# Performance work log

Measured on AMD Instinct MI355X. Metric: run time of the kernel, lower is better.

Reference implementation:

```python
import jax, jax.numpy as jnp
import numpy as np

B, C, D_MODEL, N_HEADS = 2, 2048, 1024, 16


def rotary_matrix(context_length: int, d: int) -> jnp.ndarray:
    """Faithful vectorization of get_rotary_matrix: theta = 10000^(-2*(i-1)/d)."""
    half = d // 2
    i = jnp.arange(half, dtype=jnp.float32)
    theta = 10000.0 ** (-2.0 * (i - 1.0) / d)          # note the (i-1), as in source
    m = jnp.arange(context_length, dtype=jnp.float32)
    ang = m[:, None] * theta                            # [C, d/2]
    c, s = jnp.cos(ang), jnp.sin(ang)
    ev = 2 * jnp.arange(half)
    od = ev + 1
    R = jnp.zeros((context_length, d, d), jnp.float32)
    R = R.at[:, ev, ev].set(c)
    R = R.at[:, ev, od].set(-s)
    R = R.at[:, od, ev].set(s)
    R = R.at[:, od, od].set(c)
    return R


def setup_inputs() -> dict:
    key = jax.random.key(0)
    k1, k2, k3, k4 = jax.random.split(key, 4)
    x = jax.random.normal(k1, (B, C, D_MODEL), dtype=jnp.float32)
    w_qkv = jax.random.normal(k2, (3 * D_MODEL, D_MODEL), dtype=jnp.float32) * 0.02
    w_out = jax.random.normal(k3, (D_MODEL, D_MODEL), dtype=jnp.float32) * 0.02
    b_out = jax.random.normal(k4, (D_MODEL,), dtype=jnp.float32) * 0.02
    return {"x": x, "w_qkv": w_qkv, "w_out": w_out, "b_out": b_out}


def reference(x, w_qkv, w_out, b_out):
    b, c, d = x.shape
    h = N_HEADS
    dh = d // h
    qkv = x @ w_qkv.T                                   # [B,C,3D]
    q, k, v = jnp.split(qkv, 3, axis=-1)
    # [B,C,D] -> [B,H,C,dh]
    q = q.reshape(b, c, h, dh).transpose(0, 2, 1, 3)
    k = k.reshape(b, c, h, dh).transpose(0, 2, 1, 3)
    v = v.reshape(b, c, h, dh).transpose(0, 2, 1, 3)
    R = rotary_matrix(c, dh)                            # [C,dh,dh]
    q_rot = jnp.einsum('bhci,cij->bhcj', q, R)
    k_rot = jnp.einsum('bhci,cij->bhcj', k, R)
    scale = jnp.sqrt(jnp.float32(dh))
    # exact math of the source: exp with no max subtraction, separate num/den
    attn_num = jnp.exp(jnp.einsum('bhqd,bhkd->bhqk', q_rot, k_rot) / scale)
    attn_den = jnp.exp(jnp.einsum('bhqd,bhkd->bhqk', q, k) / scale)
    attn_den = jnp.sum(attn_den, axis=-1, keepdims=True)
    attn = attn_num / attn_den
    causal = jnp.tril(jnp.ones((c, c), jnp.float32))[None, None]
    attn = jnp.where(causal == 0, 0.0, attn)
    y = jnp.einsum('bhqk,bhkd->bhqd', attn, v)
    y = y.transpose(0, 2, 1, 3).reshape(b, c, d)
    return y @ w_out.T + b_out
```

## Files before the change

### kernel.cpp

```cpp
#include <hip/hip_runtime.h>
#include <math.h>
#include <stdint.h>

#define BB 2
#define CC 2048
#define DD 1024
#define HH 16
#define DHH 64
#define HALF 32

typedef __attribute__((ext_vector_type(8))) short bf16x8;
typedef __attribute__((ext_vector_type(4))) float f32x4;
typedef unsigned int u32;

#define EXPC 0.1803368801f

__device__ __forceinline__ ushort f2bf(float f) {
    uint32_t u = __builtin_bit_cast(uint32_t, f);
    u = (u + 0x7FFFu + ((u >> 16) & 1u)) >> 16;
    return (ushort)u;
}

__device__ __forceinline__ void gload16(const void* g, void* lds) {
    __builtin_amdgcn_global_load_lds(
        (const u32 __attribute__((address_space(1)))*)g,
        (u32 __attribute__((address_space(3)))*)lds, 16, 0, 0);
}

__global__ __launch_bounds__(256) void cast3_k(const float* __restrict__ x,
                                               const float* __restrict__ wq,
                                               const float* __restrict__ wo,
                                               ushort* __restrict__ xb,
                                               ushort* __restrict__ wqb,
                                               ushort* __restrict__ wob) {
    int id = blockIdx.x * 256 + threadIdx.x;
    const float* s;
    ushort* d;
    int off;
    if (id < 524288)       { s = x;  d = xb;  off = id; }
    else if (id < 917504)  { s = wq; d = wqb; off = id - 524288; }
    else                   { s = wo; d = wob; off = id - 917504; }
    float4 a = *reinterpret_cast<const float4*>(s + (size_t)off * 8);
    float4 b = *reinterpret_cast<const float4*>(s + (size_t)off * 8 + 4);
    bf16x8 o;
    o[0] = (short)f2bf(a.x); o[1] = (short)f2bf(a.y);
    o[2] = (short)f2bf(a.z); o[3] = (short)f2bf(a.w);
    o[4] = (short)f2bf(b.x); o[5] = (short)f2bf(b.y);
    o[6] = (short)f2bf(b.z); o[7] = (short)f2bf(b.w);
    *reinterpret_cast<bf16x8*>(d + (size_t)off * 8) = o;
}

__global__ __launch_bounds__(256) void rope_table_k(float* __restrict__ ct, float* __restrict__ st) {
    int idx = blockIdx.x * 256 + threadIdx.x;
    if (idx >= CC * HALF) return;
    int m = idx >> 5;
    int t = idx & 31;
    double theta_d = pow(10000.0, -2.0 * ((double)t - 1.0) / 64.0);
    float theta = (float)theta_d;
    float ang = (float)m * theta;
    ct[idx] = cosf(ang);
    st[idx] = sinf(ang);
}

__global__ __launch_bounds__(256) void qkv_gemm_mfma_k(const ushort* __restrict__ xb,
                                                       const ushort* __restrict__ wqb,
                                                       const float* __restrict__ ct,
                                                       const float* __restrict__ st,
                                                       ushort* __restrict__ q,
                                                       ushort* __restrict__ k,
                                                       ushort* __restrict__ qr,
                                                       ushort* __restrict__ kr,
                                                       ushort* __restrict__ vT3) {
    __shared__ ushort Al[128 * 64];
    __shared__ ushort Bl[128 * 64];
    const int tid = threadIdx.x;
    const int w = tid >> 6, l = tid & 63;
    const int l15 = l & 15, lg = l >> 4;
    const int wr = w >> 1, wc = w & 1;
    const int m0 = blockIdx.x * 128, n0 = blockIdx.y * 128;
    const int lrow = l >> 3, lch = l & 7;

    f32x4 acc[4][4];
#pragma unroll
    for (int i = 0; i < 4; i++)
#pragma unroll
        for (int j = 0; j < 4; j++) acc[i][j] = (f32x4){0.f, 0.f, 0.f, 0.f};

    for (int k0 = 0; k0 < 1024; k0 += 64) {
        __syncthreads();
#pragma unroll
        for (int c = 0; c < 4; c++) {
            int row = w * 32 + c * 8 + lrow;
            int gch = (lch ^ (row & 7)) * 8;
            gload16(xb + (size_t)(m0 + row) * 1024 + k0 + gch, &Al[(w * 32 + c * 8) * 64]);
            gload16(wqb + (size_t)(n0 + row) * 1024 + k0 + gch, &Bl[(w * 32 + c * 8) * 64]);
        }
        __syncthreads();
#pragma unroll
        for (int kk = 0; kk < 2; kk++) {
            bf16x8 a[4], b[4];
#pragma unroll
            for (int mt = 0; mt < 4; mt++) {
                int row = wr * 64 + mt * 16 + l15;
                a[mt] = *reinterpret_cast<const bf16x8*>(&Al[row * 64 + ((kk * 4 + lg) ^ (row & 7)) * 8]);
            }
#pragma unroll
            for (int nt = 0; nt < 4; nt++) {
                int row = wc * 64 + nt * 16 + l15;
                b[nt] = *reinterpret_cast<const bf16x8*>(&Bl[row * 64 + ((kk * 4 + lg) ^ (row & 7)) * 8]);
            }
#pragma unroll
            for (int mt = 0; mt < 4; mt++)
#pragma unroll
                for (int nt = 0; nt < 4; nt++)
                    acc[mt][nt] = __builtin_amdgcn_mfma_f32_16x16x32_bf16(a[mt], b[nt], acc[mt][nt], 0, 0, 0);
        }
    }
#pragma unroll
    for (int mt = 0; mt < 4; mt++)
#pragma unroll
        for (int nt = 0; nt < 4; nt++) {
            int n = n0 + wc * 64 + nt * 16 + l15;
            int part = n >> 10;
            int d = n & 1023;
            int h = d >> 6, dd = d & 63;
            int mbase = m0 + wr * 64 + mt * 16 + lg * 4;
            int bb = mbase >> 11, cpos = mbase & 2047;
            if (part == 2) {
                int kt = cpos >> 6, kcol = cpos & 63;
                ushort4 pk;
                pk.x = f2bf(acc[mt][nt][0]); pk.y = f2bf(acc[mt][nt][1]);
                pk.z = f2bf(acc[mt][nt][2]); pk.w = f2bf(acc[mt][nt][3]);
                size_t off = ((((size_t)(bb * HH + h)) * 32 + kt) * 64 + dd) * 64 + kcol;
                *reinterpret_cast<ushort4*>(vT3 + off) = pk;
            } else {
                ushort* dstu = (part == 0) ? q : k;
                ushort* dstr = (part == 0) ? qr : kr;
                const float sgn = (dd & 1) ? -1.f : 1.f;
                const int t = dd >> 1;
#pragma unroll
                for (int r = 0; r < 4; r++) {
                    float val = acc[mt][nt][r];
                    float par = __shfl_xor(val, 1, 64);
                    float c = ct[(cpos + r) * 32 + t];
                    float s = st[(cpos + r) * 32 + t];
                    float rot = val * c + sgn * par * s;
                    size_t base = (((size_t)bb * HH + h) * CC + (cpos + r)) * DHH + dd;
                    dstu[base] = f2bf(val);
                    dstr[base] = f2bf(rot);
                }
            }
        }
}

__global__ __launch_bounds__(256) void den_k(const ushort* __restrict__ qg,
                                             const ushort* __restrict__ kg,
                                             float* __restrict__ deng) {
    __shared__ ushort Kd[2][128 * 64];
    const int tid = threadIdx.x;
    const int w = tid >> 6, l = tid & 63;
    const int l15 = l & 15, lg = l >> 4;
    const int lrow = l >> 3, lch = l & 7;
    const int bh = blockIdx.y;
    const int q0 = blockIdx.x * 64;
    const ushort* qb = qg + (size_t)bh * CC * DHH;
    const ushort* kb = kg + (size_t)bh * CC * DHH;

    bf16x8 qf[2];
#pragma unroll
    for (int kk = 0; kk < 2; kk++) {
        int row = q0 + w * 16 + l15;
        qf[kk] = *reinterpret_cast<const bf16x8*>(qb + (size_t)row * DHH + kk * 32 + lg * 8);
    }

    float dacc[2] = {0.f, 0.f};

#define DSTAGE(KT, BUF)                                                                     \
    {                                                                                       \
        const int sk0 = (KT) * 128;                                                         \
        _Pragma("unroll")                                                                   \
        for (int c = 0; c < 4; c++) {                                                       \
            int row = w * 32 + c * 8 + lrow;                                                \
            int gch = (lch ^ (row & 7)) * 8;                                                \
            gload16(kb + (size_t)(sk0 + row) * DHH + gch, &Kd[BUF][(w * 32 + c * 8) * 64]); \
        }                                                                                   \
    }

    DSTAGE(0, 0);
    __syncthreads();
    int cur = 0;

    for (int kt = 0; kt < 16; kt++) {
        if (kt < 15) DSTAGE(kt + 1, cur ^ 1);
#pragma unroll
        for (int nt = 0; nt < 8; nt++) {
            f32x4 s = (f32x4){0.f, 0.f, 0.f, 0.f};
#pragma unroll
            for (int kk = 0; kk < 2; kk++) {
                int krow = nt * 16 + l15;
                bf16x8 ka = *reinterpret_cast<const bf16x8*>(
                    &Kd[cur][krow * 64 + ((kk * 4 + lg) ^ (krow & 7)) * 8]);
                s = __builtin_amdgcn_mfma_f32_16x16x32_bf16(ka, qf[kk], s, 0, 0, 0);
            }
#pragma unroll
            for (int r = 0; r < 4; r++)
                dacc[nt & 1] += __builtin_amdgcn_exp2f(s[r] * EXPC);
        }
        __syncthreads();
        cur ^= 1;
    }
    float d = dacc[0] + dacc[1];
    d += __shfl_xor(d, 16, 64);
    d += __shfl_xor(d, 32, 64);
    if (lg == 0)
        deng[(size_t)bh * CC + q0 + w * 16 + l15] = d;
#undef DSTAGE
}

__global__ __launch_bounds__(256, 2) void attn_pair_k(const ushort* __restrict__ vT3,
                                                      const ushort* __restrict__ qrg,
                                                      const ushort* __restrict__ krg,
                                                      const float* __restrict__ deng,
                                                      ushort* __restrict__ y) {
    __shared__ ushort Krl[2][64 * 64];
    __shared__ ushort Pl[4][16 * 64];

    const int tid = threadIdx.x;
    const int w = tid >> 6, l = tid & 63;
    const int l15 = l & 15, lg = l >> 4;
    const int lrow = l >> 3, lch = l & 7;

    const int bid = blockIdx.x;
    const int xcd = bid & 7;
    const int idx = bid >> 3;
    const int sub = idx & 3;
    const int tp = idx >> 2;
    const int bh = xcd * 4 + sub;
    const int q0a = tp * 64;
    const int NB = 31 - tp;
    const int q0b = NB * 64;

    const ushort* qrb = qrg + (size_t)bh * CC * DHH;
    const ushort* krb = krg + (size_t)bh * CC * DHH;
    const ushort* vtb = vT3 + (size_t)bh * 32 * 64 * 64;

    bf16x8 qrfA[2], qrfB[2];
#pragma unroll
    for (int kk = 0; kk < 2; kk++) {
        qrfA[kk] = *reinterpret_cast<const bf16x8*>(qrb + (size_t)(q0a + w * 16 + l15) * DHH + kk * 32 + lg * 8);
        qrfB[kk] = *reinterpret_cast<const bf16x8*>(qrb + (size_t)(q0b + w * 16 + l15) * DHH + kk * 32 + lg * 8);
    }

    f32x4 yaccA[4], yaccB[4];
#pragma unroll
    for (int nt = 0; nt < 4; nt++) {
        yaccA[nt] = (f32x4){0.f, 0.f, 0.f, 0.f};
        yaccB[nt] = (f32x4){0.f, 0.f, 0.f, 0.f};
    }

#define STAGE(KT, BUF)                                                                         \
    {                                                                                          \
        const int sk0 = (KT) * 64;                                                             \
        _Pragma("unroll")                                                                      \
        for (int c = 0; c < 2; c++) {                                                          \
            int row = w * 16 + c * 8 + lrow;                                                   \
            int gch = (lch ^ (row & 7)) * 8;                                                   \
            gload16(krb + (size_t)(sk0 + row) * DHH + gch, &Krl[BUF][(w * 16 + c * 8) * 64]);  \
        }                                                                                      \
    }

#define NUMPV(Q0, QRF, YACC, LASTKT)                                                           \
    {                                                                                          \
        const bool diag = (kt == (LASTKT));                                                    \
        const int qrow = (Q0) + w * 16 + l15;                                                  \
        _Pragma("unroll")                                                                      \
        for (int nt = 0; nt < 4; nt++) {                                                       \
            f32x4 s = (f32x4){0.f, 0.f, 0.f, 0.f};                                             \
            _Pragma("unroll")                                                                  \
            for (int kk = 0; kk < 2; kk++) {                                                   \
                int krow = nt * 16 + l15;                                                      \
                bf16x8 ka = *reinterpret_cast<const bf16x8*>(                                  \
                    &Krl[cur][krow * 64 + ((kk * 4 + lg) ^ (krow & 7)) * 8]);                  \
                s = __builtin_amdgcn_mfma_f32_16x16x32_bf16(ka, (QRF)[kk], s, 0, 0, 0);        \
            }                                                                                  \
            float pe[4];                                                                       \
            _Pragma("unroll")                                                                  \
            for (int r = 0; r < 4; r++)                                                        \
                pe[r] = __builtin_amdgcn_exp2f(s[r] * EXPC);                                   \
            if (diag) {                                                                        \
                _Pragma("unroll")                                                              \
                for (int r = 0; r < 4; r++) {                                                  \
                    int key = kt * 64 + nt * 16 + lg * 4 + r;                                  \
                    pe[r] = (key <= qrow) ? pe[r] : 0.f;                                       \
                }                                                                              \
            }                                                                                  \
            u32 pk0, pk1;                                                                      \
            asm("v_cvt_pk_bf16_f32 %0, %1, %2" : "=v"(pk0) : "v"(pe[0]), "v"(pe[1]));          \
            asm("v_cvt_pk_bf16_f32 %0, %1, %2" : "=v"(pk1) : "v"(pe[2]), "v"(pe[3]));          \
            int swzc = (nt * 2 + (lg >> 1)) ^ (l15 & 7);                                       \
            uint2 pr; pr.x = pk0; pr.y = pk1;                                                  \
            *reinterpret_cast<uint2*>(&Pl[w][l15 * 64 + swzc * 8 + (lg & 1) * 4]) = pr;        \
        }                                                                                      \
        bf16x8 pa[2];                                                                          \
        _Pragma("unroll")                                                                      \
        for (int kk2 = 0; kk2 < 2; kk2++) {                                                    \
            int rc = (kk2 * 4 + lg) ^ (l15 & 7);                                               \
            pa[kk2] = *reinterpret_cast<const bf16x8*>(&Pl[w][l15 * 64 + rc * 8]);             \
        }                                                                                      \
        _Pragma("unroll")                                                                      \
        for (int nt2 = 0; nt2 < 4; nt2++)                                                      \
            _Pragma("unroll")                                                                  \
            for (int kk2 = 0; kk2 < 2; kk2++)                                                  \
                (YACC)[nt2] = __builtin_amdgcn_mfma_f32_16x16x32_bf16(pa[kk2], vf[nt2][kk2],   \
                                                                      (YACC)[nt2], 0, 0, 0);   \
    }

    STAGE(0, 0);
    __syncthreads();
    int cur = 0;

    for (int kt = 0; kt <= NB; kt++) {
        bf16x8 vf[4][2];
        const ushort* vt0 = vtb + (size_t)kt * 64 * 64;
#pragma unroll
        for (int nt2 = 0; nt2 < 4; nt2++)
#pragma unroll
            for (int kk2 = 0; kk2 < 2; kk2++)
                vf[nt2][kk2] = *reinterpret_cast<const bf16x8*>(
                    vt0 + (nt2 * 16 + l15) * 64 + kk2 * 32 + lg * 8);

        if (kt < NB) STAGE(kt + 1, cur ^ 1);

        if (kt <= tp) NUMPV(q0a, qrfA, yaccA, tp);
        NUMPV(q0b, qrfB, yaccB, NB);

        __syncthreads();
        cur ^= 1;
    }

    const int b = bh >> 4, h = bh & 15;
#pragma unroll
    for (int r = 0; r < 4; r++) {
        int rowA = q0a + w * 16 + lg * 4 + r;
        int rowB = q0b + w * 16 + lg * 4 + r;
        float invA = 1.f / deng[(size_t)bh * CC + rowA];
        float invB = 1.f / deng[(size_t)bh * CC + rowB];
#pragma unroll
        for (int nt2 = 0; nt2 < 4; nt2++) {
            y[((size_t)b * CC + rowA) * DD + h * DHH + nt2 * 16 + l15] = f2bf(yaccA[nt2][r] * invA);
            y[((size_t)b * CC + rowB) * DD + h * DHH + nt2 * 16 + l15] = f2bf(yaccB[nt2][r] * invB);
        }
    }
#undef STAGE
#undef NUMPV
}

__global__ __launch_bounds__(256) void out_proj_mfma_k(const ushort* __restrict__ yb,
                                                       const ushort* __restrict__ wob,
                                                       const float* __restrict__ bias,
                                                       float* __restrict__ out) {
    __shared__ ushort Al[128 * 64];
    __shared__ ushort Bl[128 * 64];
    const int tid = threadIdx.x;
    const int w = tid >> 6, l = tid & 63;
    const int l15 = l & 15, lg = l >> 4;
    const int wr = w >> 1, wc = w & 1;
    const int m0 = blockIdx.x * 128, n0 = blockIdx.y * 128;
    const int lrow = l >> 3, lch = l & 7;

    f32x4 acc[4][4];
#pragma unroll
    for (int i = 0; i < 4; i++)
#pragma unroll
        for (int j = 0; j < 4; j++) acc[i][j] = (f32x4){0.f, 0.f, 0.f, 0.f};

    for (int k0 = 0; k0 < 1024; k0 += 64) {
        __syncthreads();
#pragma unroll
        for (int c = 0; c < 4; c++) {
            int row = w * 32 + c * 8 + lrow;
            int gch = (lch ^ (row & 7)) * 8;
            gload16(yb + (size_t)(m0 + row) * 1024 + k0 + gch, &Al[(w * 32 + c * 8) * 64]);
            gload16(wob + (size_t)(n0 + row) * 1024 + k0 + gch, &Bl[(w * 32 + c * 8) * 64]);
        }
        __syncthreads();
#pragma unroll
        for (int kk = 0; kk < 2; kk++) {
            bf16x8 a[4], b[4];
#pragma unroll
            for (int mt = 0; mt < 4; mt++) {
                int row = wr * 64 + mt * 16 + l15;
                a[mt] = *reinterpret_cast<const bf16x8*>(&Al[row * 64 + ((kk * 4 + lg) ^ (row & 7)) * 8]);
            }
#pragma unroll
            for (int nt = 0; nt < 4; nt++) {
                int row = wc * 64 + nt * 16 + l15;
                b[nt] = *reinterpret_cast<const bf16x8*>(&Bl[row * 64 + ((kk * 4 + lg) ^ (row & 7)) * 8]);
            }
#pragma unroll
            for (int mt = 0; mt < 4; mt++)
#pragma unroll
                for (int nt = 0; nt < 4; nt++)
                    acc[mt][nt] = __builtin_amdgcn_mfma_f32_16x16x32_bf16(a[mt], b[nt], acc[mt][nt], 0, 0, 0);
        }
    }
#pragma unroll
    for (int mt = 0; mt < 4; mt++)
#pragma unroll
        for (int nt = 0; nt < 4; nt++) {
            int n = n0 + wc * 64 + nt * 16 + l15;
            float bv = bias[n];
#pragma unroll
            for (int r = 0; r < 4; r++) {
                int m = m0 + wr * 64 + mt * 16 + lg * 4 + r;
                out[(size_t)m * 1024 + n] = acc[mt][nt][r] + bv;
            }
        }
}

extern "C" void kernel_launch(void* const* d_in, const int* in_sizes, int n_in,
                              void* d_out, int out_size, void* d_ws, size_t ws_size,
                              hipStream_t stream) {
    (void)in_sizes; (void)n_in; (void)out_size; (void)ws_size;
    const float* x     = (const float*)d_in[0];
    const float* w_qkv = (const float*)d_in[1];
    const float* w_out = (const float*)d_in[2];
    const float* b_out = (const float*)d_in[3];
    float* out = (float*)d_out;

    char* p = (char*)d_ws;
    float* ct = (float*)p;  p += (size_t)CC * HALF * 4;
    float* st = (float*)p;  p += (size_t)CC * HALF * 4;
    ushort* xb  = (ushort*)p; p += (size_t)4096 * 1024 * 2;
    ushort* wqb = (ushort*)p; p += (size_t)3072 * 1024 * 2;
    ushort* wob = (ushort*)p; p += (size_t)1024 * 1024 * 2;
    const size_t TEN = (size_t)BB * HH * CC * DHH;
    ushort* qb = (ushort*)p; p += TEN * 2;
    ushort* kb = (ushort*)p; p += TEN * 2;
    ushort* vT = (ushort*)p; p += TEN * 2;
    ushort* qr = (ushort*)p; p += TEN * 2;
    ushort* kr = (ushort*)p; p += TEN * 2;
    ushort* yb = (ushort*)p; p += (size_t)4096 * 1024 * 2;
    float* den = (float*)p;  p += (size_t)32 * CC * 4;

    cast3_k<<<dim3(4096), dim3(256), 0, stream>>>(x, w_qkv, w_out, xb, wqb, wob);
    rope_table_k<<<dim3((CC * HALF) / 256), dim3(256), 0, stream>>>(ct, st);
    qkv_gemm_mfma_k<<<dim3(32, 24), dim3(256), 0, stream>>>(xb, wqb, ct, st, qb, kb, qr, kr, vT);
    den_k<<<dim3(32, 32), dim3(256), 0, stream>>>(qb, kb, den);
    attn_pair_k<<<dim3(512), dim3(256), 0, stream>>>(vT, qr, kr, den, yb);
    out_proj_mfma_k<<<dim3(32, 8), dim3(256), 0, stream>>>(yb, wob, b_out, out);
}
```

Before: 176.1 us.

## Fuse denominator computation into paired causal attention kernel

Removes the separate den_k kernel and computes the unmasked softmax denominator inside the attention kernel. Each block now walks all 32 key tiles, staging both unrotated K and rotated K into LDS and accumulating exp sums for both query tiles. The denominators are reduced and broadcast in registers, so no global den buffer is needed. The change also adds s_setprio around MFMA groups and raises launch bounds to 4 blocks per SM. The cost is more LDS per block, more registers and longer per-block loops.

Result: slower. 264.7 us (+50.3%).

```diff
diff --git a/kernel.cpp b/kernel.cpp
--- a/kernel.cpp
+++ b/kernel.cpp
@@ -153,75 +153,13 @@
         }
 }
 
-__global__ __launch_bounds__(256) void den_k(const ushort* __restrict__ qg,
-                                             const ushort* __restrict__ kg,
-                                             float* __restrict__ deng) {
-    __shared__ ushort Kd[2][128 * 64];
-    const int tid = threadIdx.x;
-    const int w = tid >> 6, l = tid & 63;
-    const int l15 = l & 15, lg = l >> 4;
-    const int lrow = l >> 3, lch = l & 7;
-    const int bh = blockIdx.y;
-    const int q0 = blockIdx.x * 64;
-    const ushort* qb = qg + (size_t)bh * CC * DHH;
-    const ushort* kb = kg + (size_t)bh * CC * DHH;
-
-    bf16x8 qf[2];
-#pragma unroll
-    for (int kk = 0; kk < 2; kk++) {
-        int row = q0 + w * 16 + l15;
-        qf[kk] = *reinterpret_cast<const bf16x8*>(qb + (size_t)row * DHH + kk * 32 + lg * 8);
-    }
-
-    float dacc[2] = {0.f, 0.f};
-
-#define DSTAGE(KT, BUF)                                                                     \
-    {                                                                                       \
-        const int sk0 = (KT) * 128;                                                         \
-        _Pragma("unroll")                                                                   \
-        for (int c = 0; c < 4; c++) {                                                       \
-            int row = w * 32 + c * 8 + lrow;                                                \
-            int gch = (lch ^ (row & 7)) * 8;                                                \
-            gload16(kb + (size_t)(sk0 + row) * DHH + gch, &Kd[BUF][(w * 32 + c * 8) * 64]); \
-        }                                                                                   \
-    }
-
-    DSTAGE(0, 0);
-    __syncthreads();
-    int cur = 0;
-
-    for (int kt = 0; kt < 16; kt++) {
-        if (kt < 15) DSTAGE(kt + 1, cur ^ 1);
-#pragma unroll
-        for (int nt = 0; nt < 8; nt++) {
-            f32x4 s = (f32x4){0.f, 0.f, 0.f, 0.f};
-#pragma unroll
-            for (int kk = 0; kk < 2; kk++) {
-                int krow = nt * 16 + l15;
-                bf16x8 ka = *reinterpret_cast<const bf16x8*>(
-                    &Kd[cur][krow * 64 + ((kk * 4 + lg) ^ (krow & 7)) * 8]);
-                s = __builtin_amdgcn_mfma_f32_16x16x32_bf16(ka, qf[kk], s, 0, 0, 0);
-            }
-#pragma unroll
-            for (int r = 0; r < 4; r++)
-                dacc[nt & 1] += __builtin_amdgcn_exp2f(s[r] * EXPC);
-        }
-        __syncthreads();
-        cur ^= 1;
-    }
-    float d = dacc[0] + dacc[1];
-    d += __shfl_xor(d, 16, 64);
-    d += __shfl_xor(d, 32, 64);
-    if (lg == 0)
-        deng[(size_t)bh * CC + q0 + w * 16 + l15] = d;
-#undef DSTAGE
-}
-
-__global__ __launch_bounds__(256, 2) void attn_pair_k(const ushort* __restrict__ vT3,
-                                                      const ushort* __restrict__ qrg,
-                                                      const ushort* __restrict__ krg,
-                                                      const float* __restrict__ deng,
-                                                      ushort* __restrict__ y) {
+__global__ __launch_bounds__(256, 4) void attn_fused_k(const ushort* __restrict__ vT3,
+                                                       const ushort* __restrict__ qg,
+                                                       const ushort* __restrict__ kg,
+                                                       const ushort* __restrict__ qrg,
+                                                       const ushort* __restrict__ krg,
+                                                       ushort* __restrict__ y) {
+    __shared__ ushort Kl[2][64 * 64];
     __shared__ ushort Krl[2][64 * 64];
     __shared__ ushort Pl[4][16 * 64];
 
@@ -236,19 +174,25 @@
     const int sub = idx & 3;
     const int tp = idx >> 2;
     const int bh = xcd * 4 + sub;
+    const int NB = 31 - tp;
     const int q0a = tp * 64;
-    const int NB = 31 - tp;
     const int q0b = NB * 64;
 
+    const ushort* qb  = qg  + (size_t)bh * CC * DHH;
+    const ushort* kb  = kg  + (size_t)bh * CC * DHH;
     const ushort* qrb = qrg + (size_t)bh * CC * DHH;
     const ushort* krb = krg + (size_t)bh * CC * DHH;
     const ushort* vtb = vT3 + (size_t)bh * 32 * 64 * 64;
 
-    bf16x8 qrfA[2], qrfB[2];
+    bf16x8 qfA[2], qfB[2], qrfA[2], qrfB[2];
 #pragma unroll
     for (int kk = 0; kk < 2; kk++) {
-        qrfA[kk] = *reinterpret_cast<const bf16x8*>(qrb + (size_t)(q0a + w * 16 + l15) * DHH + kk * 32 + lg * 8);
-        qrfB[kk] = *reinterpret_cast<const bf16x8*>(qrb + (size_t)(q0b + w * 16 + l15) * DHH + kk * 32 + lg * 8);
+        int ra = q0a + w * 16 + l15;
+        int rb = q0b + w * 16 + l15;
+        qfA[kk]  = *reinterpret_cast<const bf16x8*>(qb  + (size_t)ra * DHH + kk * 32 + lg * 8);
+        qfB[kk]  = *reinterpret_cast<const bf16x8*>(qb  + (size_t)rb * DHH + kk * 32 + lg * 8);
+        qrfA[kk] = *reinterpret_cast<const bf16x8*>(qrb + (size_t)ra * DHH + kk * 32 + lg * 8);
+        qrfB[kk] = *reinterpret_cast<const bf16x8*>(qrb + (size_t)rb * DHH + kk * 32 + lg * 8);
     }
 
     f32x4 yaccA[4], yaccB[4];
@@ -257,6 +201,7 @@
         yaccA[nt] = (f32x4){0.f, 0.f, 0.f, 0.f};
         yaccB[nt] = (f32x4){0.f, 0.f, 0.f, 0.f};
     }
+    float daccA0 = 0.f, daccA1 = 0.f, daccB0 = 0.f, daccB1 = 0.f;
 
 #define STAGE(KT, BUF)                                                                         \
     {                                                                                          \
@@ -265,7 +210,9 @@
         for (int c = 0; c < 2; c++) {                                                          \
             int row = w * 16 + c * 8 + lrow;                                                   \
             int gch = (lch ^ (row & 7)) * 8;                                                   \
-            gload16(krb + (size_t)(sk0 + row) * DHH + gch, &Krl[BUF][(w * 16 + c * 8) * 64]);  \
+            gload16(kb + (size_t)(sk0 + row) * DHH + gch, &Kl[BUF][(w * 16 + c * 8) * 64]);    \
+            if ((KT) <= NB)                                                                    \
+                gload16(krb + (size_t)(sk0 + row) * DHH + gch, &Krl[BUF][(w * 16 + c * 8) * 64]); \
         }                                                                                      \
     }
 
@@ -275,14 +222,17 @@
         const int qrow = (Q0) + w * 16 + l15;                                                  \
         _Pragma("unroll")                                                                      \
         for (int nt = 0; nt < 4; nt++) {                                                       \
+            bf16x8 kra0, kra1;                                                                 \
+            {                                                                                  \
+                int krow = nt * 16 + l15;                                                      \
+                kra0 = *reinterpret_cast<const bf16x8*>(&Krl[cur][krow * 64 + ((0 + lg) ^ (krow & 7)) * 8]); \
+                kra1 = *reinterpret_cast<const bf16x8*>(&Krl[cur][krow * 64 + ((4 + lg) ^ (krow & 7)) * 8]); \
+            }                                                                                  \
+            __builtin_amdgcn_s_setprio(1);                                                     \
             f32x4 s = (f32x4){0.f, 0.f, 0.f, 0.f};                                             \
-            _Pragma("unroll")                                                                  \
-            for (int kk = 0; kk < 2; kk++) {                                                   \
-                int krow = nt * 16 + l15;                                                      \
-                bf16x8 ka = *reinterpret_cast<const bf16x8*>(                                  \
-                    &Krl[cur][krow * 64 + ((kk * 4 + lg) ^ (krow & 7)) * 8]);                  \
-                s = __builtin_amdgcn_mfma_f32_16x16x32_bf16(ka, (QRF)[kk], s, 0, 0, 0);        \
-            }                                                                                  \
+            s = __builtin_amdgcn_mfma_f32_16x16x32_bf16(kra0, (QRF)[0], s, 0, 0, 0);           \
+            s = __builtin_amdgcn_mfma_f32_16x16x32_bf16(kra1, (QRF)[1], s, 0, 0, 0);           \
+            __builtin_amdgcn_s_setprio(0);                                                     \
             float pe[4];                                                                       \
             _Pragma("unroll")                                                                  \
             for (int r = 0; r < 4; r++)                                                        \
@@ -307,44 +257,89 @@
             int rc = (kk2 * 4 + lg) ^ (l15 & 7);                                               \
             pa[kk2] = *reinterpret_cast<const bf16x8*>(&Pl[w][l15 * 64 + rc * 8]);             \
         }                                                                                      \
+        __builtin_amdgcn_s_setprio(1);                                                         \
         _Pragma("unroll")                                                                      \
-        for (int nt2 = 0; nt2 < 4; nt2++)                                                      \
-            _Pragma("unroll")                                                                  \
-            for (int kk2 = 0; kk2 < 2; kk2++)                                                  \
-                (YACC)[nt2] = __builtin_amdgcn_mfma_f32_16x16x32_bf16(pa[kk2], vf[nt2][kk2],   \
-                                                                      (YACC)[nt2], 0, 0, 0);   \
+        for (int nt2 = 0; nt2 < 4; nt2++) {                                                    \
+            (YACC)[nt2] = __builtin_amdgcn_mfma_f32_16x16x32_bf16(pa[0], vf[nt2][0], (YACC)[nt2], 0, 0, 0); \
+            (YACC)[nt2] = __builtin_amdgcn_mfma_f32_16x16x32_bf16(pa[1], vf[nt2][1], (YACC)[nt2], 0, 0, 0); \
+        }                                                                                      \
+        __builtin_amdgcn_s_setprio(0);                                                         \
     }
 
     STAGE(0, 0);
     __syncthreads();
     int cur = 0;
 
-    for (int kt = 0; kt <= NB; kt++) {
+    for (int kt = 0; kt < 32; kt++) {
+        const bool actA = (kt <= tp);
+        const bool actB = (kt <= NB);
+
         bf16x8 vf[4][2];
-        const ushort* vt0 = vtb + (size_t)kt * 64 * 64;
-#pragma unroll
-        for (int nt2 = 0; nt2 < 4; nt2++)
-#pragma unroll
-            for (int kk2 = 0; kk2 < 2; kk2++)
-                vf[nt2][kk2] = *reinterpret_cast<const bf16x8*>(
-                    vt0 + (nt2 * 16 + l15) * 64 + kk2 * 32 + lg * 8);
-
-        if (kt < NB) STAGE(kt + 1, cur ^ 1);
-
-        if (kt <= tp) NUMPV(q0a, qrfA, yaccA, tp);
-        NUMPV(q0b, qrfB, yaccB, NB);
+        if (actB) {
+            const ushort* vt0 = vtb + (size_t)kt * 64 * 64;
+#pragma unroll
+            for (int nt2 = 0; nt2 < 4; nt2++)
+#pragma unroll
+                for (int kk2 = 0; kk2 < 2; kk2++)
+                    vf[nt2][kk2] = *reinterpret_cast<const bf16x8*>(
+                        vt0 + (nt2 * 16 + l15) * 64 + kk2 * 32 + lg * 8);
+        }
+
+        if (kt + 1 < 32) STAGE(kt + 1, cur ^ 1);
+
+#pragma unroll
+        for (int nt = 0; nt < 4; nt++) {
+            bf16x8 ka0, ka1;
+            {
+                int krow = nt * 16 + l15;
+                ka0 = *reinterpret_cast<const bf16x8*>(&Kl[cur][krow * 64 + ((0 + lg) ^ (krow & 7)) * 8]);
+                ka1 = *reinterpret_cast<const bf16x8*>(&Kl[cur][krow * 64 + ((4 + lg) ^ (krow & 7)) * 8]);
+            }
+            __builtin_amdgcn_s_setprio(1);
+            f32x4 sA = (f32x4){0.f, 0.f, 0.f, 0.f};
+            sA = __builtin_amdgcn_mfma_f32_16x16x32_bf16(ka0, qfA[0], sA, 0, 0, 0);
+            sA = __builtin_amdgcn_mfma_f32_16x16x32_bf16(ka1, qfA[1], sA, 0, 0, 0);
+            f32x4 sB = (f32x4){0.f, 0.f, 0.f, 0.f};
+            sB = __builtin_amdgcn_mfma_f32_16x16x32_bf16(ka0, qfB[0], sB, 0, 0, 0);
+            sB = __builtin_amdgcn_mfma_f32_16x16x32_bf16(ka1, qfB[1], sB, 0, 0, 0);
+            __builtin_amdgcn_s_setprio(0);
+            if (nt & 1) {
+#pragma unroll
+                for (int r = 0; r < 4; r++) {
+                    daccA1 += __builtin_amdgcn_exp2f(sA[r] * EXPC);
+                    daccB1 += __builtin_amdgcn_exp2f(sB[r] * EXPC);
+                }
+            } else {
+#pragma unroll
+                for (int r = 0; r < 4; r++) {
+                    daccA0 += __builtin_amdgcn_exp2f(sA[r] * EXPC);
+                    daccB0 += __builtin_amdgcn_exp2f(sB[r] * EXPC);
+                }
+            }
+        }
+
+        if (actB) NUMPV(q0b, qrfB, yaccB, NB);
+        if (actA) NUMPV(q0a, qrfA, yaccA, tp);
 
         __syncthreads();
         cur ^= 1;
     }
 
+    float denA = daccA0 + daccA1, denB = daccB0 + daccB1;
+    denA += __shfl_xor(denA, 16, 64);
+    denA += __shfl_xor(denA, 32, 64);
+    denB += __shfl_xor(denB, 16, 64);
+    denB += __shfl_xor(denB, 32, 64);
+
     const int b = bh >> 4, h = bh & 15;
 #pragma unroll
     for (int r = 0; r < 4; r++) {
+        float drA = __shfl(denA, lg * 4 + r, 64);
+        float drB = __shfl(denB, lg * 4 + r, 64);
+        float invA = 1.f / drA;
+        float invB = 1.f / drB;
         int rowA = q0a + w * 16 + lg * 4 + r;
         int rowB = q0b + w * 16 + lg * 4 + r;
-        float invA = 1.f / deng[(size_t)bh * CC + rowA];
-        float invB = 1.f / deng[(size_t)bh * CC + rowB];
 #pragma unroll
         for (int nt2 = 0; nt2 < 4; nt2++) {
             y[((size_t)b * CC + rowA) * DD + h * DHH + nt2 * 16 + l15] = f2bf(yaccA[nt2][r] * invA);
@@ -441,12 +436,10 @@
     ushort* qr = (ushort*)p; p += TEN * 2;
     ushort* kr = (ushort*)p; p += TEN * 2;
     ushort* yb = (ushort*)p; p += (size_t)4096 * 1024 * 2;
-    float* den = (float*)p;  p += (size_t)32 * CC * 4;
 
     cast3_k<<<dim3(4096), dim3(256), 0, stream>>>(x, w_qkv, w_out, xb, wqb, wob);
     rope_table_k<<<dim3((CC * HALF) / 256), dim3(256), 0, stream>>>(ct, st);
     qkv_gemm_mfma_k<<<dim3(32, 24), dim3(256), 0, stream>>>(xb, wqb, ct, st, qb, kb, qr, kr, vT);
-    den_k<<<dim3(32, 32), dim3(256), 0, stream>>>(qb, kb, den);
-    attn_pair_k<<<dim3(512), dim3(256), 0, stream>>>(vT, qr, kr, den, yb);
+    attn_fused_k<<<dim3(512), dim3(256), 0, stream>>>(vT, qb, kb, qr, kr, yb);
     out_proj_mfma_k<<<dim3(32, 8), dim3(256), 0, stream>>>(yb, wob, b_out, out);
 }
```
